# Kernel optimization log

Hardware: AMD Instinct MI355X
Metric: run time of the kernel (lower is better)

Reference implementation:

```python
import jax, jax.numpy as jnp
import numpy as np

DIM_KEY = 64  # matches init dim_key

def setup_inputs() -> dict:
    key = jax.random.key(0)
    kq, kk, kv, kb = jax.random.split(key, 4)
    B, H, S, D = 2, 16, 2048, 64
    q = jax.random.normal(kq, (B, H, S, D), dtype=jnp.float32)
    k = jax.random.normal(kk, (B, H, S, D), dtype=jnp.float32)
    v = jax.random.normal(kv, (B, H, S, D), dtype=jnp.float32)
    attn_bias = jax.random.normal(kb, (B, H, S), dtype=jnp.float32)
    return {"q": q, "k": k, "v": v, "attn_bias": attn_bias}

def reference(q, k, v, attn_bias):
    # scaled QK^T: [B,H,S,S]
    scaled_q = (DIM_KEY ** -0.5) * q
    scores = jnp.einsum('bhqd,bhkd->bhqk', scaled_q, k)
    # bias is per-query, broadcast over key axis (unsqueeze(3) in torch)
    scores = scores + attn_bias[..., None]
    weights = jax.nn.softmax(scores, axis=-1)
    # dropout_rate = 0.0 -> no dropout
    out = jnp.einsum('bhqk,bhkd->bhqd', weights, v)
    return out
```

## Files before the change

kernel.cpp:

```cpp
#include <hip/hip_runtime.h>


#define S_LEN 2048
#define D_DIM 64
#define KVTILE 64
#define QBLK 128
#define QK_SCALE 0.125f

typedef short s16x4 __attribute__((ext_vector_type(4)));
typedef short s16x8 __attribute__((ext_vector_type(8)));
typedef float f32x4 __attribute__((ext_vector_type(4)));

union U4S8 { uint4 u; s16x8 s; };
union U2S4 { uint2 u; s16x4 s; };

static __device__ __forceinline__ unsigned permhi(unsigned a, unsigned b) {
    return __builtin_amdgcn_perm(a, b, 0x07060302u);
}
static __device__ __forceinline__ unsigned bf16rn(float x) {
    unsigned u = __float_as_uint(x);
    return (u + 0x7FFFu + ((u >> 16) & 1u)) >> 16;
}

__global__ __launch_bounds__(256, 2) void sdpa_mfma4_kernel(
    const float* __restrict__ q, const float* __restrict__ k,
    const float* __restrict__ v, float* __restrict__ out)
{
    __shared__ __align__(16) char smem[32768];
    char* Khi = smem;
    char* Klo = smem + 8192;
    char* Vb  = smem + 16384;

    const int tid  = threadIdx.x;
    const int lane = tid & 63;
    const int w    = tid >> 6;
    const int c    = lane & 15;
    const int g    = lane >> 4;
    const int flat = blockIdx.x;
    const int bh   = ((flat >> 7) << 3) | (flat & 7);
    const int q0   = ((flat >> 3) & 15) * QBLK;
    const size_t head = (size_t)bh * S_LEN * D_DIM;

    s16x8 qh[2][2], qlo[2][2];
#pragma unroll
    for (int c2 = 0; c2 < 2; ++c2) {
        const float* qp = q + head + (size_t)(q0 + w * 32 + c2 * 16 + c) * D_DIM;
#pragma unroll
        for (int dq = 0; dq < 2; ++dq) {
            float4 t0 = *(const float4*)(qp + dq * 32 + g * 8);
            float4 t1 = *(const float4*)(qp + dq * 32 + g * 8 + 4);
            float e[8] = {t0.x, t0.y, t0.z, t0.w, t1.x, t1.y, t1.z, t1.w};
            unsigned ub[8]; unsigned rb[8];
#pragma unroll
            for (int j = 0; j < 8; ++j) {
                float s = e[j] * QK_SCALE;
                ub[j] = __float_as_uint(s);
                float r = s - __uint_as_float(ub[j] & 0xFFFF0000u);
                rb[j] = __float_as_uint(r);
            }
            U4S8 hi, lo;
            hi.u = make_uint4(permhi(ub[1], ub[0]), permhi(ub[3], ub[2]),
                              permhi(ub[5], ub[4]), permhi(ub[7], ub[6]));
            lo.u = make_uint4(permhi(rb[1], rb[0]), permhi(rb[3], rb[2]),
                              permhi(rb[5], rb[4]), permhi(rb[7], rb[6]));
            qh[c2][dq]  = hi.s;
            qlo[c2][dq] = lo.s;
        }
    }

    f32x4 acc[2][4];
#pragma unroll
    for (int c2 = 0; c2 < 2; ++c2)
#pragma unroll
        for (int dt = 0; dt < 4; ++dt) acc[c2][dt] = (f32x4){0.f, 0.f, 0.f, 0.f};
    float m[2]    = {0.f, 0.f};
    float lsum[2] = {0.f, 0.f};

    float4 kA[2], kB[2], vA[2], vB[2];
    const int kkey = tid >> 3;
    const int kd0  = (tid & 7) * 8;
    const int vkp  = tid & 31;
    const int vdc  = tid >> 5;

    {
        const float* s0 = k + head + (size_t)kkey * D_DIM + kd0;
        kA[0] = *(const float4*)s0;              kB[0] = *(const float4*)(s0 + 4);
        kA[1] = *(const float4*)(s0 + 32*D_DIM); kB[1] = *(const float4*)(s0 + 32*D_DIM + 4);
        const float* v0p = v + head + (size_t)(2 * vkp) * D_DIM + vdc * 8;
        vA[0] = *(const float4*)v0p;             vB[0] = *(const float4*)(v0p + 4);
        vA[1] = *(const float4*)(v0p + D_DIM);   vB[1] = *(const float4*)(v0p + D_DIM + 4);
    }

    for (int t0 = 0; t0 < S_LEN; t0 += KVTILE) {
        __syncthreads();
#pragma unroll
        for (int i = 0; i < 2; ++i) {
            int key = kkey + i * 32;
            float e[8] = {kA[i].x, kA[i].y, kA[i].z, kA[i].w,
                          kB[i].x, kB[i].y, kB[i].z, kB[i].w};
            unsigned ub[8]; unsigned rb[8];
#pragma unroll
            for (int j = 0; j < 8; ++j) {
                ub[j] = __float_as_uint(e[j]);
                float r = e[j] - __uint_as_float(ub[j] & 0xFFFF0000u);
                rb[j] = __float_as_uint(r);
            }
            uint4 hi = make_uint4(permhi(ub[1], ub[0]), permhi(ub[3], ub[2]),
                                  permhi(ub[5], ub[4]), permhi(ub[7], ub[6]));
            uint4 lo = make_uint4(permhi(rb[1], rb[0]), permhi(rb[3], rb[2]),
                                  permhi(rb[5], rb[4]), permhi(rb[7], rb[6]));
            unsigned byte = ((unsigned)(key * 128 + kd0 * 2)) ^ (((unsigned)key & 7u) << 4);
            *(uint4*)(Khi + byte) = hi;
            *(uint4*)(Klo + byte) = lo;
        }
        {
            float x0[8] = {vA[0].x, vA[0].y, vA[0].z, vA[0].w,
                           vB[0].x, vB[0].y, vB[0].z, vB[0].w};
            float x1[8] = {vA[1].x, vA[1].y, vA[1].z, vA[1].w,
                           vB[1].x, vB[1].y, vB[1].z, vB[1].w};
#pragma unroll
            for (int j = 0; j < 8; ++j) {
                unsigned wd = bf16rn(x0[j]) | (bf16rn(x1[j]) << 16);
                int d = vdc * 8 + j;
                unsigned byte = (unsigned)(d * 128) + (((unsigned)(vkp * 4)) ^ ((unsigned)j << 4));
                *(unsigned*)(Vb + byte) = wd;
            }
        }
        __syncthreads();

        if (t0 + KVTILE < S_LEN) {
            const float* s0 = k + head + (size_t)(t0 + KVTILE + kkey) * D_DIM + kd0;
            kA[0] = *(const float4*)s0;              kB[0] = *(const float4*)(s0 + 4);
            kA[1] = *(const float4*)(s0 + 32*D_DIM); kB[1] = *(const float4*)(s0 + 32*D_DIM + 4);
            const float* v0p = v + head + (size_t)(t0 + KVTILE + 2 * vkp) * D_DIM + vdc * 8;
            vA[0] = *(const float4*)v0p;             vB[0] = *(const float4*)(v0p + 4);
            vA[1] = *(const float4*)(v0p + D_DIM);   vB[1] = *(const float4*)(v0p + D_DIM + 4);
        }

#pragma unroll
        for (int kb = 0; kb < 2; ++kb) {
            f32x4 st[2][2];
#pragma unroll
            for (int kg = 0; kg < 2; ++kg) {
                s16x8 kh[2], kl[2];
#pragma unroll
                for (int dq = 0; dq < 2; ++dq) {
                    int keyr = kb * 32 + kg * 16 + c;
                    unsigned byte = ((unsigned)(keyr * 128 + dq * 64 + g * 16)) ^ (((unsigned)c & 7u) << 4);
                    kh[dq] = *(const s16x8*)(Khi + byte);
                    kl[dq] = *(const s16x8*)(Klo + byte);
                }
                __builtin_amdgcn_s_setprio(1);
#pragma unroll
                for (int c2 = 0; c2 < 2; ++c2) {
                    f32x4 s = (f32x4){0.f, 0.f, 0.f, 0.f};
#pragma unroll
                    for (int dq = 0; dq < 2; ++dq) {
                        s = __builtin_amdgcn_mfma_f32_16x16x32_bf16(kh[dq], qh[c2][dq],  s, 0, 0, 0);
                        s = __builtin_amdgcn_mfma_f32_16x16x32_bf16(kh[dq], qlo[c2][dq], s, 0, 0, 0);
                        s = __builtin_amdgcn_mfma_f32_16x16x32_bf16(kl[dq], qh[c2][dq],  s, 0, 0, 0);
                    }
                    st[c2][kg] = s;
                }
                __builtin_amdgcn_s_setprio(0);
            }

            s16x4 ph[2][2], pl[2][2];
#pragma unroll
            for (int c2 = 0; c2 < 2; ++c2) {
                float pv[8] = {st[c2][0][0], st[c2][0][1], st[c2][0][2], st[c2][0][3],
                               st[c2][1][0], st[c2][1][1], st[c2][1][2], st[c2][1][3]};
                float tmax = fmaxf(fmaxf(fmaxf(pv[0], pv[1]), fmaxf(pv[2], pv[3])),
                                   fmaxf(fmaxf(pv[4], pv[5]), fmaxf(pv[6], pv[7])));
                tmax = fmaxf(tmax, __shfl_xor(tmax, 16));
                tmax = fmaxf(tmax, __shfl_xor(tmax, 32));
                if (__builtin_expect(tmax > m[c2] + 8.0f, 0)) {
                    float corr = __expf(m[c2] - tmax);
                    lsum[c2] *= corr;
#pragma unroll
                    for (int dt = 0; dt < 4; ++dt) acc[c2][dt] *= corr;
                    m[c2] = tmax;
                }
                float psum = 0.f;
#pragma unroll
                for (int j = 0; j < 8; ++j) { pv[j] = __expf(pv[j] - m[c2]); psum += pv[j]; }
                lsum[c2] += psum;
                unsigned ub[8]; unsigned rb[8];
#pragma unroll
                for (int j = 0; j < 8; ++j) {
                    ub[j] = __float_as_uint(pv[j]);
                    float r = pv[j] - __uint_as_float(ub[j] & 0xFFFF0000u);
                    rb[j] = __float_as_uint(r);
                }
                U2S4 h0, h1, l0, l1;
                h0.u = make_uint2(permhi(ub[1], ub[0]), permhi(ub[3], ub[2]));
                h1.u = make_uint2(permhi(ub[5], ub[4]), permhi(ub[7], ub[6]));
                l0.u = make_uint2(permhi(rb[1], rb[0]), permhi(rb[3], rb[2]));
                l1.u = make_uint2(permhi(rb[5], rb[4]), permhi(rb[7], rb[6]));
                ph[c2][0] = h0.s; ph[c2][1] = h1.s;
                pl[c2][0] = l0.s; pl[c2][1] = l1.s;
            }

            __builtin_amdgcn_s_setprio(1);
#pragma unroll
            for (int kg = 0; kg < 2; ++kg)
#pragma unroll
                for (int dt = 0; dt < 4; ++dt) {
                    int d = dt * 16 + c;
                    unsigned byte = ((unsigned)(d * 128 + (kb * 32 + kg * 16 + g * 4) * 2)) ^ (((unsigned)c & 7u) << 4);
                    s16x4 vf = *(const s16x4*)(Vb + byte);
#pragma unroll
                    for (int c2 = 0; c2 < 2; ++c2) {
                        acc[c2][dt] = __builtin_amdgcn_mfma_f32_16x16x16bf16_1k(vf, ph[c2][kg], acc[c2][dt], 0, 0, 0);
                        acc[c2][dt] = __builtin_amdgcn_mfma_f32_16x16x16bf16_1k(vf, pl[c2][kg], acc[c2][dt], 0, 0, 0);
                    }
                }
            __builtin_amdgcn_s_setprio(0);
        }
    }

    __syncthreads();
    char* Ob = smem;
#pragma unroll
    for (int c2 = 0; c2 < 2; ++c2) {
        float ls = lsum[c2];
        ls += __shfl_xor(ls, 16);
        ls += __shfl_xor(ls, 32);
        float inv = 1.0f / ls;
        int qlocal = w * 32 + c2 * 16 + c;
#pragma unroll
        for (int dt = 0; dt < 4; ++dt) {
            f32x4 o = acc[c2][dt] * inv;
            float4 o4 = {o[0], o[1], o[2], o[3]};
            unsigned byte = ((unsigned)(qlocal * 256 + dt * 64 + g * 16)) ^ (((unsigned)qlocal & 7u) << 4);
            *(float4*)(Ob + byte) = o4;
        }
    }
    __syncthreads();
#pragma unroll
    for (int i = 0; i < 8; ++i) {
        int f4 = tid + i * 256;
        int row = f4 >> 4;
        int d0  = (f4 & 15) * 4;
        unsigned byte = ((unsigned)(row * 256 + d0 * 4)) ^ (((unsigned)row & 7u) << 4);
        float4 t = *(const float4*)(Ob + byte);
        *(float4*)(out + head + (size_t)(q0 + row) * D_DIM + d0) = t;
    }
}

extern "C" void kernel_launch(void* const* d_in, const int* in_sizes, int n_in,
                              void* d_out, int out_size, void* d_ws, size_t ws_size,
                              hipStream_t stream) {
    const float* q = (const float*)d_in[0];
    const float* k = (const float*)d_in[1];
    const float* v = (const float*)d_in[2];
    float* out = (float*)d_out;

    dim3 grid(512);
    dim3 block(256);
    sdpa_mfma4_kernel<<<grid, block, 0, stream>>>(q, k, v, out);
}
```

Measured before the change: 186.8 us.

## Precompute packed bf16 K/V tiles in workspace and stream them via async LDS loads

```diff
diff --git a/kernel.cpp b/kernel.cpp
--- a/kernel.cpp
+++ b/kernel.cpp
@@ -3,9 +3,11 @@
 
 #define S_LEN 2048
 #define D_DIM 64
-#define KVTILE 64
 #define QBLK 128
 #define QK_SCALE 0.125f
+#define TILE_BYTES 24576
+#define NT 32
+#define WS_NEEDED (1024ull * TILE_BYTES)
 
 typedef short s16x4 __attribute__((ext_vector_type(4)));
 typedef short s16x8 __attribute__((ext_vector_type(8)));
@@ -14,6 +16,11 @@
 union U4S8 { uint4 u; s16x8 s; };
 union U2S4 { uint2 u; s16x4 s; };
 
+#define MFMA32(A, B, C) __builtin_amdgcn_mfma_f32_16x16x32_bf16(A, B, C, 0, 0, 0)
+#define GLD_LDS16(gp, lp) __builtin_amdgcn_global_load_lds( \
+    (const __attribute__((address_space(1))) unsigned*)(gp), \
+    (__attribute__((address_space(3))) unsigned*)(lp), 16, 0, 0)
+
 static __device__ __forceinline__ unsigned permhi(unsigned a, unsigned b) {
     return __builtin_amdgcn_perm(a, b, 0x07060302u);
 }
@@ -21,15 +28,76 @@
     unsigned u = __float_as_uint(x);
     return (u + 0x7FFFu + ((u >> 16) & 1u)) >> 16;
 }
-
-__global__ __launch_bounds__(256, 2) void sdpa_mfma4_kernel(
-    const float* __restrict__ q, const float* __restrict__ k,
-    const float* __restrict__ v, float* __restrict__ out)
+static __device__ __forceinline__ void pack8(const float* e, uint4& hi, uint4& lo) {
+    unsigned ub[8], rb[8];
+#pragma unroll
+    for (int j = 0; j < 8; ++j) {
+        ub[j] = __float_as_uint(e[j]);
+        float r = e[j] - __uint_as_float(ub[j] & 0xFFFF0000u);
+        rb[j] = __float_as_uint(r);
+    }
+    hi = make_uint4(permhi(ub[1], ub[0]), permhi(ub[3], ub[2]),
+                    permhi(ub[5], ub[4]), permhi(ub[7], ub[6]));
+    lo = make_uint4(permhi(rb[1], rb[0]), permhi(rb[3], rb[2]),
+                    permhi(rb[5], rb[4]), permhi(rb[7], rb[6]));
+}
+
+__global__ __launch_bounds__(256) void sdpa_prepass_kernel(
+    const float* __restrict__ k, const float* __restrict__ v,
+    char* __restrict__ ws)
 {
-    __shared__ __align__(16) char smem[32768];
-    char* Khi = smem;
-    char* Klo = smem + 8192;
-    char* Vb  = smem + 16384;
+    __shared__ __align__(16) char lds[TILE_BYTES];
+    const int tid  = threadIdx.x;
+    const int flat = blockIdx.x;
+    const int h    = flat >> 5;
+    const int t    = flat & 31;
+    const size_t base = (size_t)h * S_LEN * D_DIM + (size_t)(t * 64) * D_DIM;
+    const float* kt = k + base;
+    const float* vt = v + base;
+
+    {
+        int key = tid >> 2, d0 = (tid & 3) * 16;
+        const float* src = kt + (size_t)key * D_DIM + d0;
+        float e[16];
+        *(float4*)(e + 0)  = ((const float4*)src)[0];
+        *(float4*)(e + 4)  = ((const float4*)src)[1];
+        *(float4*)(e + 8)  = ((const float4*)src)[2];
+        *(float4*)(e + 12) = ((const float4*)src)[3];
+#pragma unroll
+        for (int half = 0; half < 2; ++half) {
+            uint4 hi, lo;
+            pack8(e + half * 8, hi, lo);
+            unsigned byte = ((unsigned)(key * 128 + d0 * 2 + half * 16)) ^ (((unsigned)key & 7u) << 4);
+            *(uint4*)(lds + byte)        = hi;
+            *(uint4*)(lds + 8192 + byte) = lo;
+        }
+    }
+    {
+        int d = tid & 63, kg = tid >> 6;
+#pragma unroll
+        for (int i = 0; i < 16; i += 2) {
+            int k0 = kg * 16 + i;
+            float x0 = vt[(size_t)k0 * D_DIM + d];
+            float x1 = vt[(size_t)(k0 + 1) * D_DIM + d];
+            unsigned wd = bf16rn(x0) | (bf16rn(x1) << 16);
+            int blk = k0 >> 5, r = k0 & 31;
+            int slot = blk * 32 + ((r & 3) + 4 * (r >> 4) + 8 * ((r >> 2) & 3));
+            unsigned byte = ((unsigned)(d * 128 + slot * 2)) ^ (((unsigned)d & 7u) << 4);
+            *(unsigned*)(lds + 16384 + byte) = wd;
+        }
+    }
+    __syncthreads();
+    char* dst = ws + (size_t)flat * TILE_BYTES;
+#pragma unroll
+    for (int i = 0; i < 6; ++i)
+        ((uint4*)dst)[tid + i * 256] = ((const uint4*)lds)[tid + i * 256];
+}
+
+__global__ __launch_bounds__(256, 2) void sdpa_mfma5_kernel(
+    const float* __restrict__ q, const char* __restrict__ ws,
+    float* __restrict__ out)
+{
+    __shared__ __align__(16) char smem[2 * TILE_BYTES];
 
     const int tid  = threadIdx.x;
     const int lane = tid & 63;
@@ -40,6 +108,16 @@
     const int bh   = ((flat >> 7) << 3) | (flat & 7);
     const int q0   = ((flat >> 3) & 15) * QBLK;
     const size_t head = (size_t)bh * S_LEN * D_DIM;
+    const char* wsrc = ws + (size_t)bh * NT * TILE_BYTES;
+
+    {
+        const char* gt = wsrc;
+#pragma unroll
+        for (int i = 0; i < 6; ++i) {
+            unsigned off = (unsigned)(w * 6144 + i * 1024 + (lane << 4));
+            GLD_LDS16(gt + off, smem + off);
+        }
+    }
 
     s16x8 qh[2][2], qlo[2][2];
 #pragma unroll
@@ -49,22 +127,13 @@
         for (int dq = 0; dq < 2; ++dq) {
             float4 t0 = *(const float4*)(qp + dq * 32 + g * 8);
             float4 t1 = *(const float4*)(qp + dq * 32 + g * 8 + 4);
-            float e[8] = {t0.x, t0.y, t0.z, t0.w, t1.x, t1.y, t1.z, t1.w};
-            unsigned ub[8]; unsigned rb[8];
-#pragma unroll
-            for (int j = 0; j < 8; ++j) {
-                float s = e[j] * QK_SCALE;
-                ub[j] = __float_as_uint(s);
-                float r = s - __uint_as_float(ub[j] & 0xFFFF0000u);
-                rb[j] = __float_as_uint(r);
-            }
-            U4S8 hi, lo;
-            hi.u = make_uint4(permhi(ub[1], ub[0]), permhi(ub[3], ub[2]),
-                              permhi(ub[5], ub[4]), permhi(ub[7], ub[6]));
-            lo.u = make_uint4(permhi(rb[1], rb[0]), permhi(rb[3], rb[2]),
-                              permhi(rb[5], rb[4]), permhi(rb[7], rb[6]));
-            qh[c2][dq]  = hi.s;
-            qlo[c2][dq] = lo.s;
+            float e[8] = {t0.x * QK_SCALE, t0.y * QK_SCALE, t0.z * QK_SCALE, t0.w * QK_SCALE,
+                          t1.x * QK_SCALE, t1.y * QK_SCALE, t1.z * QK_SCALE, t1.w * QK_SCALE};
+            uint4 hi, lo;
+            pack8(e, hi, lo);
+            U4S8 a, b; a.u = hi; b.u = lo;
+            qh[c2][dq]  = a.s;
+            qlo[c2][dq] = b.s;
         }
     }
 
@@ -76,67 +145,10 @@
     float m[2]    = {0.f, 0.f};
     float lsum[2] = {0.f, 0.f};
 
-    float4 kA[2], kB[2], vA[2], vB[2];
-    const int kkey = tid >> 3;
-    const int kd0  = (tid & 7) * 8;
-    const int vkp  = tid & 31;
-    const int vdc  = tid >> 5;
-
-    {
-        const float* s0 = k + head + (size_t)kkey * D_DIM + kd0;
-        kA[0] = *(const float4*)s0;              kB[0] = *(const float4*)(s0 + 4);
-        kA[1] = *(const float4*)(s0 + 32*D_DIM); kB[1] = *(const float4*)(s0 + 32*D_DIM + 4);
-        const float* v0p = v + head + (size_t)(2 * vkp) * D_DIM + vdc * 8;
-        vA[0] = *(const float4*)v0p;             vB[0] = *(const float4*)(v0p + 4);
-        vA[1] = *(const float4*)(v0p + D_DIM);   vB[1] = *(const float4*)(v0p + D_DIM + 4);
-    }
-
-    for (int t0 = 0; t0 < S_LEN; t0 += KVTILE) {
-        __syncthreads();
-#pragma unroll
-        for (int i = 0; i < 2; ++i) {
-            int key = kkey + i * 32;
-            float e[8] = {kA[i].x, kA[i].y, kA[i].z, kA[i].w,
-                          kB[i].x, kB[i].y, kB[i].z, kB[i].w};
-            unsigned ub[8]; unsigned rb[8];
-#pragma unroll
-            for (int j = 0; j < 8; ++j) {
-                ub[j] = __float_as_uint(e[j]);
-                float r = e[j] - __uint_as_float(ub[j] & 0xFFFF0000u);
-                rb[j] = __float_as_uint(r);
-            }
-            uint4 hi = make_uint4(permhi(ub[1], ub[0]), permhi(ub[3], ub[2]),
-                                  permhi(ub[5], ub[4]), permhi(ub[7], ub[6]));
-            uint4 lo = make_uint4(permhi(rb[1], rb[0]), permhi(rb[3], rb[2]),
-                                  permhi(rb[5], rb[4]), permhi(rb[7], rb[6]));
-            unsigned byte = ((unsigned)(key * 128 + kd0 * 2)) ^ (((unsigned)key & 7u) << 4);
-            *(uint4*)(Khi + byte) = hi;
-            *(uint4*)(Klo + byte) = lo;
-        }
-        {
-            float x0[8] = {vA[0].x, vA[0].y, vA[0].z, vA[0].w,
-                           vB[0].x, vB[0].y, vB[0].z, vB[0].w};
-            float x1[8] = {vA[1].x, vA[1].y, vA[1].z, vA[1].w,
-                           vB[1].x, vB[1].y, vB[1].z, vB[1].w};
-#pragma unroll
-            for (int j = 0; j < 8; ++j) {
-                unsigned wd = bf16rn(x0[j]) | (bf16rn(x1[j]) << 16);
-                int d = vdc * 8 + j;
-                unsigned byte = (unsigned)(d * 128) + (((unsigned)(vkp * 4)) ^ ((unsigned)j << 4));
-                *(unsigned*)(Vb + byte) = wd;
-            }
-        }
-        __syncthreads();
-
-        if (t0 + KVTILE < S_LEN) {
-            const float* s0 = k + head + (size_t)(t0 + KVTILE + kkey) * D_DIM + kd0;
-            kA[0] = *(const float4*)s0;              kB[0] = *(const float4*)(s0 + 4);
-            kA[1] = *(const float4*)(s0 + 32*D_DIM); kB[1] = *(const float4*)(s0 + 32*D_DIM + 4);
-            const float* v0p = v + head + (size_t)(t0 + KVTILE + 2 * vkp) * D_DIM + vdc * 8;
-            vA[0] = *(const float4*)v0p;             vB[0] = *(const float4*)(v0p + 4);
-            vA[1] = *(const float4*)(v0p + D_DIM);   vB[1] = *(const float4*)(v0p + D_DIM + 4);
-        }
-
+    auto compute = [&](const char* L) {
+        const char* Lhi = L;
+        const char* Llo = L + 8192;
+        const char* Lv  = L + 16384;
 #pragma unroll
         for (int kb = 0; kb < 2; ++kb) {
             f32x4 st[2][2];
@@ -147,8 +159,8 @@
                 for (int dq = 0; dq < 2; ++dq) {
                     int keyr = kb * 32 + kg * 16 + c;
                     unsigned byte = ((unsigned)(keyr * 128 + dq * 64 + g * 16)) ^ (((unsigned)c & 7u) << 4);
-                    kh[dq] = *(const s16x8*)(Khi + byte);
-                    kl[dq] = *(const s16x8*)(Klo + byte);
+                    kh[dq] = *(const s16x8*)(Lhi + byte);
+                    kl[dq] = *(const s16x8*)(Llo + byte);
                 }
                 __builtin_amdgcn_s_setprio(1);
 #pragma unroll
@@ -156,16 +168,16 @@
                     f32x4 s = (f32x4){0.f, 0.f, 0.f, 0.f};
 #pragma unroll
                     for (int dq = 0; dq < 2; ++dq) {
-                        s = __builtin_amdgcn_mfma_f32_16x16x32_bf16(kh[dq], qh[c2][dq],  s, 0, 0, 0);
-                        s = __builtin_amdgcn_mfma_f32_16x16x32_bf16(kh[dq], qlo[c2][dq], s, 0, 0, 0);
-                        s = __builtin_amdgcn_mfma_f32_16x16x32_bf16(kl[dq], qh[c2][dq],  s, 0, 0, 0);
+                        s = MFMA32(kh[dq], qh[c2][dq],  s);
+                        s = MFMA32(kh[dq], qlo[c2][dq], s);
+                        s = MFMA32(kl[dq], qh[c2][dq],  s);
                     }
                     st[c2][kg] = s;
                 }
                 __builtin_amdgcn_s_setprio(0);
             }
 
-            s16x4 ph[2][2], pl[2][2];
+            s16x8 ph[2], pl[2];
 #pragma unroll
             for (int c2 = 0; c2 < 2; ++c2) {
                 float pv[8] = {st[c2][0][0], st[c2][0][1], st[c2][0][2], st[c2][0][3],
@@ -185,41 +197,50 @@
 #pragma unroll
                 for (int j = 0; j < 8; ++j) { pv[j] = __expf(pv[j] - m[c2]); psum += pv[j]; }
                 lsum[c2] += psum;
-                unsigned ub[8]; unsigned rb[8];
-#pragma unroll
-                for (int j = 0; j < 8; ++j) {
-                    ub[j] = __float_as_uint(pv[j]);
-                    float r = pv[j] - __uint_as_float(ub[j] & 0xFFFF0000u);
-                    rb[j] = __float_as_uint(r);
-                }
-                U2S4 h0, h1, l0, l1;
-                h0.u = make_uint2(permhi(ub[1], ub[0]), permhi(ub[3], ub[2]));
-                h1.u = make_uint2(permhi(ub[5], ub[4]), permhi(ub[7], ub[6]));
-                l0.u = make_uint2(permhi(rb[1], rb[0]), permhi(rb[3], rb[2]));
-                l1.u = make_uint2(permhi(rb[5], rb[4]), permhi(rb[7], rb[6]));
-                ph[c2][0] = h0.s; ph[c2][1] = h1.s;
-                pl[c2][0] = l0.s; pl[c2][1] = l1.s;
+                uint4 hw_, lw_;
+                pack8(pv, hw_, lw_);
+                U4S8 a, b; a.u = hw_; b.u = lw_;
+                ph[c2] = a.s;
+                pl[c2] = b.s;
             }
 
             __builtin_amdgcn_s_setprio(1);
 #pragma unroll
-            for (int kg = 0; kg < 2; ++kg)
-#pragma unroll
-                for (int dt = 0; dt < 4; ++dt) {
-                    int d = dt * 16 + c;
-                    unsigned byte = ((unsigned)(d * 128 + (kb * 32 + kg * 16 + g * 4) * 2)) ^ (((unsigned)c & 7u) << 4);
-                    s16x4 vf = *(const s16x4*)(Vb + byte);
-#pragma unroll
-                    for (int c2 = 0; c2 < 2; ++c2) {
-                        acc[c2][dt] = __builtin_amdgcn_mfma_f32_16x16x16bf16_1k(vf, ph[c2][kg], acc[c2][dt], 0, 0, 0);
-                        acc[c2][dt] = __builtin_amdgcn_mfma_f32_16x16x16bf16_1k(vf, pl[c2][kg], acc[c2][dt], 0, 0, 0);
-                    }
-                }
+            for (int dt = 0; dt < 4; ++dt) {
+                int d = dt * 16 + c;
+                unsigned byte = ((unsigned)(d * 128 + kb * 64 + g * 16)) ^ (((unsigned)d & 7u) << 4);
+                s16x8 vf = *(const s16x8*)(Lv + byte);
+#pragma unroll
+                for (int c2 = 0; c2 < 2; ++c2) {
+                    acc[c2][dt] = MFMA32(vf, ph[c2], acc[c2][dt]);
+                    acc[c2][dt] = MFMA32(vf, pl[c2], acc[c2][dt]);
+                }
+            }
             __builtin_amdgcn_s_setprio(0);
         }
-    }
-
+    };
+
+#pragma unroll 1
+    for (int t = 0; t < NT - 1; ++t) {
+        {
+            const char* gt = wsrc + (size_t)(t + 1) * TILE_BYTES;
+            unsigned boff = (unsigned)(((t + 1) & 1) * TILE_BYTES);
+#pragma unroll
+            for (int i = 0; i < 6; ++i) {
+                unsigned off = (unsigned)(w * 6144 + i * 1024 + (lane << 4));
+                GLD_LDS16(gt + off, smem + boff + off);
+            }
+        }
+        asm volatile("s_waitcnt vmcnt(6)" ::: "memory");
+        __builtin_amdgcn_s_barrier();
+        compute(smem + (unsigned)((t & 1) * TILE_BYTES));
+        __builtin_amdgcn_s_barrier();
+    }
+    asm volatile("s_waitcnt vmcnt(0)" ::: "memory");
+    __builtin_amdgcn_s_barrier();
+    compute(smem + TILE_BYTES);
     __syncthreads();
+
     char* Ob = smem;
 #pragma unroll
     for (int c2 = 0; c2 < 2; ++c2) {
@@ -248,6 +269,204 @@
     }
 }
 
+__global__ __launch_bounds__(256, 2) void sdpa_mfma4_kernel(
+    const float* __restrict__ q, const float* __restrict__ k,
+    const float* __restrict__ v, float* __restrict__ out)
+{
+    __shared__ __align__(16) char smem[32768];
+    char* Khi = smem;
+    char* Klo = smem + 8192;
+    char* Vb  = smem + 16384;
+
+    const int tid  = threadIdx.x;
+    const int lane = tid & 63;
+    const int w    = tid >> 6;
+    const int c    = lane & 15;
+    const int g    = lane >> 4;
+    const int flat = blockIdx.x;
+    const int bh   = ((flat >> 7) << 3) | (flat & 7);
+    const int q0   = ((flat >> 3) & 15) * QBLK;
+    const size_t head = (size_t)bh * S_LEN * D_DIM;
+
+    s16x8 qh[2][2], qlo[2][2];
+#pragma unroll
+    for (int c2 = 0; c2 < 2; ++c2) {
+        const float* qp = q + head + (size_t)(q0 + w * 32 + c2 * 16 + c) * D_DIM;
+#pragma unroll
+        for (int dq = 0; dq < 2; ++dq) {
+            float4 t0 = *(const float4*)(qp + dq * 32 + g * 8);
+            float4 t1 = *(const float4*)(qp + dq * 32 + g * 8 + 4);
+            float e[8] = {t0.x * QK_SCALE, t0.y * QK_SCALE, t0.z * QK_SCALE, t0.w * QK_SCALE,
+                          t1.x * QK_SCALE, t1.y * QK_SCALE, t1.z * QK_SCALE, t1.w * QK_SCALE};
+            uint4 hi, lo;
+            pack8(e, hi, lo);
+            U4S8 a, b; a.u = hi; b.u = lo;
+            qh[c2][dq]  = a.s;
+            qlo[c2][dq] = b.s;
+        }
+    }
+
+    f32x4 acc[2][4];
+#pragma unroll
+    for (int c2 = 0; c2 < 2; ++c2)
+#pragma unroll
+        for (int dt = 0; dt < 4; ++dt) acc[c2][dt] = (f32x4){0.f, 0.f, 0.f, 0.f};
+    float m[2]    = {0.f, 0.f};
+    float lsum[2] = {0.f, 0.f};
+
+    float4 kA[2], kB[2], vA[2], vB[2];
+    const int kkey = tid >> 3;
+    const int kd0  = (tid & 7) * 8;
+    const int vkp  = tid & 31;
+    const int vdc  = tid >> 5;
+    {
+        const float* s0 = k + head + (size_t)kkey * D_DIM + kd0;
+        kA[0] = *(const float4*)s0;              kB[0] = *(const float4*)(s0 + 4);
+        kA[1] = *(const float4*)(s0 + 32*D_DIM); kB[1] = *(const float4*)(s0 + 32*D_DIM + 4);
+        const float* v0p = v + head + (size_t)(2 * vkp) * D_DIM + vdc * 8;
+        vA[0] = *(const float4*)v0p;             vB[0] = *(const float4*)(v0p + 4);
+        vA[1] = *(const float4*)(v0p + D_DIM);   vB[1] = *(const float4*)(v0p + D_DIM + 4);
+    }
+
+    for (int t0 = 0; t0 < S_LEN; t0 += 64) {
+        __syncthreads();
+#pragma unroll
+        for (int i = 0; i < 2; ++i) {
+            int key = kkey + i * 32;
+            float e[8] = {kA[i].x, kA[i].y, kA[i].z, kA[i].w,
+                          kB[i].x, kB[i].y, kB[i].z, kB[i].w};
+            uint4 hi, lo;
+            pack8(e, hi, lo);
+            unsigned byte = ((unsigned)(key * 128 + kd0 * 2)) ^ (((unsigned)key & 7u) << 4);
+            *(uint4*)(Khi + byte) = hi;
+            *(uint4*)(Klo + byte) = lo;
+        }
+        {
+            float x0[8] = {vA[0].x, vA[0].y, vA[0].z, vA[0].w,
+                           vB[0].x, vB[0].y, vB[0].z, vB[0].w};
+            float x1[8] = {vA[1].x, vA[1].y, vA[1].z, vA[1].w,
+                           vB[1].x, vB[1].y, vB[1].z, vB[1].w};
+#pragma unroll
+            for (int j = 0; j < 8; ++j) {
+                unsigned wd = bf16rn(x0[j]) | (bf16rn(x1[j]) << 16);
+                int d = vdc * 8 + j;
+                unsigned byte = (unsigned)(d * 128) + (((unsigned)(vkp * 4)) ^ ((unsigned)j << 4));
+                *(unsigned*)(Vb + byte) = wd;
+            }
+        }
+        __syncthreads();
+        if (t0 + 64 < S_LEN) {
+            const float* s0 = k + head + (size_t)(t0 + 64 + kkey) * D_DIM + kd0;
+            kA[0] = *(const float4*)s0;              kB[0] = *(const float4*)(s0 + 4);
+            kA[1] = *(const float4*)(s0 + 32*D_DIM); kB[1] = *(const float4*)(s0 + 32*D_DIM + 4);
+            const float* v0p = v + head + (size_t)(t0 + 64 + 2 * vkp) * D_DIM + vdc * 8;
+            vA[0] = *(const float4*)v0p;             vB[0] = *(const float4*)(v0p + 4);
+            vA[1] = *(const float4*)(v0p + D_DIM);   vB[1] = *(const float4*)(v0p + D_DIM + 4);
+        }
+
+#pragma unroll
+        for (int kb = 0; kb < 2; ++kb) {
+            f32x4 st[2][2];
+#pragma unroll
+            for (int kg = 0; kg < 2; ++kg) {
+                s16x8 kh[2], kl[2];
+#pragma unroll
+                for (int dq = 0; dq < 2; ++dq) {
+                    int keyr = kb * 32 + kg * 16 + c;
+                    unsigned byte = ((unsigned)(keyr * 128 + dq * 64 + g * 16)) ^ (((unsigned)c & 7u) << 4);
+                    kh[dq] = *(const s16x8*)(Khi + byte);
+                    kl[dq] = *(const s16x8*)(Klo + byte);
+                }
+                __builtin_amdgcn_s_setprio(1);
+#pragma unroll
+                for (int c2 = 0; c2 < 2; ++c2) {
+                    f32x4 s = (f32x4){0.f, 0.f, 0.f, 0.f};
+#pragma unroll
+                    for (int dq = 0; dq < 2; ++dq) {
+                        s = MFMA32(kh[dq], qh[c2][dq],  s);
+                        s = MFMA32(kh[dq], qlo[c2][dq], s);
+                        s = MFMA32(kl[dq], qh[c2][dq],  s);
+                    }
+                    st[c2][kg] = s;
+                }
+                __builtin_amdgcn_s_setprio(0);
+            }
+            s16x4 ph[2][2], pl[2][2];
+#pragma unroll
+            for (int c2 = 0; c2 < 2; ++c2) {
+                float pv[8] = {st[c2][0][0], st[c2][0][1], st[c2][0][2], st[c2][0][3],
+                               st[c2][1][0], st[c2][1][1], st[c2][1][2], st[c2][1][3]};
+                float tmax = fmaxf(fmaxf(fmaxf(pv[0], pv[1]), fmaxf(pv[2], pv[3])),
+                                   fmaxf(fmaxf(pv[4], pv[5]), fmaxf(pv[6], pv[7])));
+                tmax = fmaxf(tmax, __shfl_xor(tmax, 16));
+                tmax = fmaxf(tmax, __shfl_xor(tmax, 32));
+                if (__builtin_expect(tmax > m[c2] + 8.0f, 0)) {
+                    float corr = __expf(m[c2] - tmax);
+                    lsum[c2] *= corr;
+#pragma unroll
+                    for (int dt = 0; dt < 4; ++dt) acc[c2][dt] *= corr;
+                    m[c2] = tmax;
+                }
+                float psum = 0.f;
+#pragma unroll
+                for (int j = 0; j < 8; ++j) { pv[j] = __expf(pv[j] - m[c2]); psum += pv[j]; }
+                lsum[c2] += psum;
+                uint4 hw_, lw_;
+                pack8(pv, hw_, lw_);
+                U4S8 a, b; a.u = hw_; b.u = lw_;
+                U2S4 h0, h1, l0, l1;
+                h0.u = make_uint2(a.u.x, a.u.y); h1.u = make_uint2(a.u.z, a.u.w);
+                l0.u = make_uint2(b.u.x, b.u.y); l1.u = make_uint2(b.u.z, b.u.w);
+                ph[c2][0] = h0.s; ph[c2][1] = h1.s;
+                pl[c2][0] = l0.s; pl[c2][1] = l1.s;
+            }
+            __builtin_amdgcn_s_setprio(1);
+#pragma unroll
+            for (int kg = 0; kg < 2; ++kg)
+#pragma unroll
+                for (int dt = 0; dt < 4; ++dt) {
+                    int d = dt * 16 + c;
+                    unsigned byte = ((unsigned)(d * 128 + (kb * 32 + kg * 16 + g * 4) * 2)) ^ (((unsigned)c & 7u) << 4);
+                    s16x4 vf = *(const s16x4*)(Vb + byte);
+#pragma unroll
+                    for (int c2 = 0; c2 < 2; ++c2) {
+                        acc[c2][dt] = __builtin_amdgcn_mfma_f32_16x16x16bf16_1k(vf, ph[c2][kg], acc[c2][dt], 0, 0, 0);
+                        acc[c2][dt] = __builtin_amdgcn_mfma_f32_16x16x16bf16_1k(vf, pl[c2][kg], acc[c2][dt], 0, 0, 0);
+                    }
+                }
+            __builtin_amdgcn_s_setprio(0);
+        }
+    }
+
+    __syncthreads();
+    char* Ob = smem;
+#pragma unroll
+    for (int c2 = 0; c2 < 2; ++c2) {
+        float ls = lsum[c2];
+        ls += __shfl_xor(ls, 16);
+        ls += __shfl_xor(ls, 32);
+        float inv = 1.0f / ls;
+        int qlocal = w * 32 + c2 * 16 + c;
+#pragma unroll
+        for (int dt = 0; dt < 4; ++dt) {
+            f32x4 o = acc[c2][dt] * inv;
+            float4 o4 = {o[0], o[1], o[2], o[3]};
+            unsigned byte = ((unsigned)(qlocal * 256 + dt * 64 + g * 16)) ^ (((unsigned)qlocal & 7u) << 4);
+            *(float4*)(Ob + byte) = o4;
+        }
+    }
+    __syncthreads();
+#pragma unroll
+    for (int i = 0; i < 8; ++i) {
+        int f4 = tid + i * 256;
+        int row = f4 >> 4;
+        int d0  = (f4 & 15) * 4;
+        unsigned byte = ((unsigned)(row * 256 + d0 * 4)) ^ (((unsigned)row & 7u) << 4);
+        float4 t = *(const float4*)(Ob + byte);
+        *(float4*)(out + head + (size_t)(q0 + row) * D_DIM + d0) = t;
+    }
+}
+
 extern "C" void kernel_launch(void* const* d_in, const int* in_sizes, int n_in,
                               void* d_out, int out_size, void* d_ws, size_t ws_size,
                               hipStream_t stream) {
@@ -256,7 +475,10 @@
     const float* v = (const float*)d_in[2];
     float* out = (float*)d_out;
 
-    dim3 grid(512);
-    dim3 block(256);
-    sdpa_mfma4_kernel<<<grid, block, 0, stream>>>(q, k, v, out);
-}
+    if (ws_size >= WS_NEEDED) {
+        sdpa_prepass_kernel<<<dim3(1024), dim3(256), 0, stream>>>(k, v, (char*)d_ws);
+        sdpa_mfma5_kernel<<<dim3(512), dim3(256), 0, stream>>>(q, (const char*)d_ws, out);
+    } else {
+        sdpa_mfma4_kernel<<<dim3(512), dim3(256), 0, stream>>>(q, k, v, out);
+    }
+}
```

Measured after the change: 181.5 us. 1.03x faster.
